# Kernel optimization log

Measured on AMD Instinct MI355X. Metric: run time of the kernel, lower is better.

Reference implementation:

```python
import jax, jax.numpy as jnp
import numpy as np

N, E, IN_DIM, HID, HEADS, OUT_DIM, T = 50000, 200000, 32, 64, 4, 32, 3
NEG_SLOPE = 0.2  # PyG GATv2Conv default


def setup_inputs() -> dict:
    key = jax.random.key(0)
    ks = jax.random.split(key, 16)
    s = 0.1
    return {
        "feat": jax.random.normal(ks[0], (N, IN_DIM), jnp.float32),
        "W_in": jax.random.normal(ks[1], (IN_DIM, HID), jnp.float32) * s,
        "b_in": jnp.zeros((HID,), jnp.float32),
        "Wl": jax.random.normal(ks[2], (2 * HID, HEADS * HID), jnp.float32) * s,
        "bl": jnp.zeros((HEADS * HID,), jnp.float32),
        "Wr": jax.random.normal(ks[3], (2 * HID, HEADS * HID), jnp.float32) * s,
        "br": jnp.zeros((HEADS * HID,), jnp.float32),
        "att": jax.random.normal(ks[4], (HEADS, HID), jnp.float32) * s,
        "b_conv": jnp.zeros((HEADS * HID,), jnp.float32),
        "Wg": jax.random.normal(ks[5], (HID, OUT_DIM), jnp.float32) * s,
        "bg": jnp.zeros((OUT_DIM,), jnp.float32),
        "edge_index": jax.random.randint(ks[6], (2, E), 0, N, jnp.int32),
        "node_mask": jax.random.randint(ks[7], (N,), 0, T + 1, jnp.int32),
        "current_state": jax.random.randint(ks[8], (N,), 0, 2, jnp.int32),
    }


def reference(feat, W_in, b_in, Wl, bl, Wr, br, att, b_conv, Wg, bg,
              edge_index, node_mask, current_state):
    # add self loops (GATv2Conv add_self_loops=True)
    loops = jnp.arange(N, dtype=edge_index.dtype)
    src = jnp.concatenate([edge_index[0], loops])  # [E+N]
    dst = jnp.concatenate([edge_index[1], loops])

    h0 = feat @ W_in + b_in  # [N, HID]
    bias_sum = b_conv.reshape(HEADS, HID).sum(0)  # heads are summed after bias add

    def step(h, i):
        active = node_mask > i  # [N] bool: nodes updated at this step
        x = jnp.concatenate([h, h0], axis=-1)  # [N, 2*HID]
        xl = (x @ Wl + bl).reshape(N, HEADS, HID)  # source transform
        xr = (x @ Wr + br).reshape(N, HEADS, HID)  # target transform
        e_act = active[src] & active[dst]  # edge alive iff both endpoints active
        s = jax.nn.leaky_relu(xl[src] + xr[dst], NEG_SLOPE)  # [E+N, H, C]
        score = jnp.einsum('ehc,hc->eh', s, att)  # [E+N, H]
        score = jnp.where(e_act[:, None], score, -1e30)
        smax = jax.lax.stop_gradient(
            jax.ops.segment_max(score, dst, num_segments=N))  # [N, H]
        ex = jnp.exp(score - smax[dst]) * e_act[:, None].astype(score.dtype)
        denom = jax.ops.segment_sum(ex, dst, num_segments=N)  # [N, H]
        alpha = ex / jnp.maximum(denom[dst], 1e-16)  # segment softmax per dst
        msg = alpha[:, :, None] * xl[src]  # [E+N, H, C]
        agg = jax.ops.segment_sum(msg, dst, num_segments=N)  # [N, H, C]
        out = jnp.tanh(agg.sum(1) + bias_sum)  # sum over heads, then Tanh
        return jnp.where(active[:, None], out, h), None

    h, _ = jax.lax.scan(step, h0, jnp.arange(T))
    # original returns g_embed(h[current_state]); fixed-shape variant: mask rows
    out = (h @ Wg + bg) * (current_state[:, None] > 0).astype(h.dtype)
    return out
```

## Files before the change

### kernel.cpp

```cpp
#include <hip/hip_runtime.h>
#include <hip/hip_bf16.h>

#define NN      50000
#define EE      200000
#define IN_DIM  32
#define HID     64
#define HEADS   4
#define OUTD    32
#define TSTEPS  3

typedef unsigned short bf16_t;
typedef __attribute__((ext_vector_type(8))) short  short8;
typedef __attribute__((ext_vector_type(4))) float  floatx4;

__device__ __forceinline__ float b2f(bf16_t u) {
    union { unsigned int i; float f; } v; v.i = ((unsigned int)u) << 16; return v.f;
}
__device__ __forceinline__ bf16_t f2b(float f) {
    union { float f; unsigned int i; } v; v.f = f;
    unsigned int r = v.i + 0x7FFF + ((v.i >> 16) & 1);
    return (bf16_t)(r >> 16);
}

__global__ __launch_bounds__(256) void k_setup(
        const void* W_in, const void* b_in, const void* att, const void* bconv,
        const void* Wg, const void* bg,
        const void* Wl_raw, const void* Wr_raw, const void* bl_raw, const void* br_raw,
        float* Winf, float* binf, float* attf, float* bcf, float* Wgf, float* bgf,
        bf16_t* __restrict__ Wt, float* __restrict__ bb,
        int* __restrict__ deg, int* __restrict__ flag, int* __restrict__ mbuf) {
    __shared__ int bad;
    int t = threadIdx.x, bid = blockIdx.x;
    if (t == 0) bad = 0;
    __syncthreads();
    {
        const bf16_t* p = (const bf16_t*)W_in;
        int mybad = 0;
        for (int i = t; i < IN_DIM * HID; i += 256) {
            float v = b2f(p[i]);
            if (v != v || fabsf(v) > 100.f) mybad = 1;
        }
        if (mybad) atomicOr(&bad, 1);
    }
    __syncthreads();
    int f = bad ? 0 : 1;
    if (bid == 0 && t == 0) *flag = f;

    if (bid < 256) {
        int i = bid * 256 + t;
        int n = i >> 7, k = i & 127;
        const void* W = (n < 256) ? Wl_raw : Wr_raw;
        int nn = (n < 256) ? n : n - 256;
        float v = f ? b2f(((const bf16_t*)W)[k * 256 + nn])
                    : ((const float*)W)[k * 256 + nn];
        Wt[i] = f2b(v);
        if (k == 0) {
            const void* b = (n < 256) ? bl_raw : br_raw;
            bb[n] = f ? b2f(((const bf16_t*)b)[nn]) : ((const float*)b)[nn];
        }
    } else if (bid < 275) {
        int i = (bid - 256) * 256 + t;
        const void* src; float* dst; int off;
        if      (i < 2048) { src = W_in;  dst = Winf; off = i; }
        else if (i < 2112) { src = b_in;  dst = binf; off = i - 2048; }
        else if (i < 2368) { src = att;   dst = attf; off = i - 2112; }
        else if (i < 2624) { src = bconv; dst = bcf;  off = i - 2368; }
        else if (i < 4672) { src = Wg;    dst = Wgf;  off = i - 2624; }
        else if (i < 4704) { src = bg;    dst = bgf;  off = i - 4672; }
        else return;
        dst[off] = f ? b2f(((const bf16_t*)src)[off]) : ((const float*)src)[off];
    } else {
        int i = (bid - 275) * 256 + t;
        if (i < NN) deg[i] = 0;
        if (bid == 275 && t < 16) mbuf[t] = 0;
    }
}

__global__ __launch_bounds__(256) void k_hist_all(const int* __restrict__ dst,
                                                  const int* __restrict__ mask,
                                                  int* __restrict__ deg,
                                                  int* __restrict__ mbuf) {
    int t = threadIdx.x, bid = blockIdx.x;
    int i = bid * 256 + t;
    if (i < EE) atomicAdd(&deg[dst[i]], 1);
    if (bid < (NN + 255) / 256) {
        __shared__ int wcnt[4][4];
        int wid = t >> 6, lane = t & 63;
        int ni = bid * 256 + t;
        bool valid = ni < NN;
        int v = 0;
        if (valid) { int m = mask[ni]; v = m < 0 ? 0 : (m > 3 ? 3 : m); }
#pragma unroll
        for (int b = 0; b < 4; b++) {
            unsigned long long mm = __ballot(valid && v == b);
            if (lane == 0) wcnt[wid][b] = __popcll(mm);
        }
        __syncthreads();
        if (t < 4) {
            int s = wcnt[0][t] + wcnt[1][t] + wcnt[2][t] + wcnt[3][t];
            if (s) atomicAdd(&mbuf[t], s);
        }
    }
}

__global__ __launch_bounds__(256) void k_scan_partial(const int* __restrict__ deg,
                                                      int* __restrict__ part, int n) {
    __shared__ int sd[256];
    int t = threadIdx.x;
    int base = blockIdx.x * 1024;
    int s = 0;
#pragma unroll
    for (int j = 0; j < 4; j++) {
        int i = base + t * 4 + j;
        if (i < n) s += deg[i];
    }
    sd[t] = s; __syncthreads();
    for (int off = 128; off > 0; off >>= 1) {
        if (t < off) sd[t] += sd[t + off];
        __syncthreads();
    }
    if (t == 0) part[blockIdx.x] = sd[0];
}

__global__ void k_scan_mid(int* part, int nch, int* mbuf) {
    if (threadIdx.x == 0 && blockIdx.x == 0) {
        int acc = 0;
        for (int i = 0; i < nch; i++) { int v = part[i]; part[i] = acc; acc += v; }
        part[nch] = acc;
        int c1 = mbuf[1], c2 = mbuf[2], c3 = mbuf[3];
        mbuf[7] = 0;
        mbuf[6] = c3;
        mbuf[5] = c3 + c2;
        mbuf[4] = c3 + c2 + c1;
        mbuf[8] = c3 + c2 + c1;
        mbuf[9] = c3 + c2;
        mbuf[10] = c3;
    }
}

__global__ __launch_bounds__(256) void k_scan_final(const int* __restrict__ deg,
                                                    const int* __restrict__ part,
                                                    int* __restrict__ row_ptr,
                                                    int* __restrict__ cursor,
                                                    int n, int nch) {
    __shared__ int sc[256];
    int t = threadIdx.x;
    int base = blockIdx.x * 1024;
    int v[4]; int s = 0;
#pragma unroll
    for (int j = 0; j < 4; j++) {
        int i = base + t * 4 + j;
        v[j] = (i < n) ? deg[i] : 0;
        s += v[j];
    }
    sc[t] = s; __syncthreads();
    for (int off = 1; off < 256; off <<= 1) {
        int add = (t >= off) ? sc[t - off] : 0;
        __syncthreads();
        sc[t] += add;
        __syncthreads();
    }
    int run = sc[t] - s + part[blockIdx.x];
#pragma unroll
    for (int j = 0; j < 4; j++) {
        int i = base + t * 4 + j;
        if (i < n) { row_ptr[i] = run; cursor[i] = run; run += v[j]; }
    }
    if (blockIdx.x == 0 && t == 0) row_ptr[n] = part[nch];
}

__global__ __launch_bounds__(256) void k_scatter_all(const int* __restrict__ src,
                                                     const int* __restrict__ dst,
                                                     int* __restrict__ cursor,
                                                     int* __restrict__ col,
                                                     const int* __restrict__ mask,
                                                     int* __restrict__ mbuf,
                                                     int* __restrict__ order) {
    int t = threadIdx.x, bid = blockIdx.x;
    int i = bid * 256 + t;
    if (i < EE) {
        int sv = src[i];
        int m = mask[sv]; m = m < 0 ? 0 : (m > 3 ? 3 : m);
        int d = dst[i];
        int pos = atomicAdd(&cursor[d], 1);
        col[pos] = sv | (m << 28);
    }
    if (bid < (NN + 255) / 256) {
        __shared__ int wcnt[4][4];
        __shared__ int bbase[4];
        int wid = t >> 6, lane = t & 63;
        int ni = bid * 256 + t;
        bool valid = ni < NN;
        int v = 0;
        if (valid) { int m = mask[ni]; v = m < 0 ? 0 : (m > 3 ? 3 : m); }
        int rank = 0;
#pragma unroll
        for (int b = 0; b < 4; b++) {
            unsigned long long mm = __ballot(valid && v == b);
            if (valid && v == b)
                rank = __popcll(mm & ((lane == 0) ? 0ull : (~0ull >> (64 - lane))));
            if (lane == 0) wcnt[wid][b] = __popcll(mm);
        }
        __syncthreads();
        if (t < 4) {
            int tot = wcnt[0][t] + wcnt[1][t] + wcnt[2][t] + wcnt[3][t];
            bbase[t] = atomicAdd(&mbuf[4 + t], tot);
        }
        __syncthreads();
        if (valid) {
            int wpre = 0;
            for (int ww = 0; ww < wid; ww++) wpre += wcnt[ww][v];
            order[bbase[v] + wpre + rank] = ni;
        }
    }
}

__global__ __launch_bounds__(256) void k_h0(const void* __restrict__ feat_raw,
                                            const float* __restrict__ W_in,
                                            const float* __restrict__ b_in,
                                            bf16_t* __restrict__ h0,
                                            bf16_t* __restrict__ h,
                                            const int* __restrict__ flag) {
    __shared__ float Ws[IN_DIM * HID];
    __shared__ float bs[HID];
    int t = threadIdx.x;
    for (int i = t; i < IN_DIM * HID; i += 256) Ws[i] = W_in[i];
    if (t < HID) bs[t] = b_in[t];
    __syncthreads();
    int node = blockIdx.x * 4 + (t >> 6);
    int c = t & 63;
    if (node >= NN) return;
    int f = *flag;
    float acc = bs[c];
    if (f) {
        const bf16_t* fr = (const bf16_t*)feat_raw + (size_t)node * IN_DIM;
#pragma unroll
        for (int k = 0; k < IN_DIM; k++) acc += b2f(fr[k]) * Ws[k * HID + c];
    } else {
        const float* fr = (const float*)feat_raw + (size_t)node * IN_DIM;
#pragma unroll
        for (int k = 0; k < IN_DIM; k++) acc += fr[k] * Ws[k * HID + c];
    }
    bf16_t o = f2b(acc);
    h0[(size_t)node * HID + c] = o;
    h [(size_t)node * HID + c] = o;
}

__global__ __launch_bounds__(256) void k_gemm_mfma(const bf16_t* __restrict__ h,
                                                   const bf16_t* __restrict__ h0,
                                                   const bf16_t* __restrict__ Wt,
                                                   const float* __restrict__ bb,
                                                   bf16_t* __restrict__ xl,
                                                   bf16_t* __restrict__ xr,
                                                   const int* __restrict__ order,
                                                   const int* __restrict__ mbuf,
                                                   int step) {
    int count = mbuf[8 + step];
    int mbase = blockIdx.x * 64;
    if (mbase >= count) return;

    __shared__ bf16_t smem[64 * 136 + 128 * 136];
    bf16_t* As = smem;
    bf16_t* Bs = smem + 64 * 136;
    bf16_t* Cs = smem;

    int t = threadIdx.x;
    int nbase = blockIdx.y * 128;

    {
        int ln = t >> 2, lq = t & 3;
        int idx = mbase + ln;
        int node = (idx < count) ? order[idx] : -1;
        ulonglong2 z; z.x = 0; z.y = 0;
#pragma unroll
        for (int j = 0; j < 2; j++) {
            int chunk = lq + j * 4;
            ulonglong2 vh = z, vh0 = z;
            if (node >= 0) {
                vh  = *(const ulonglong2*)(h  + (size_t)node * HID + chunk * 8);
                vh0 = *(const ulonglong2*)(h0 + (size_t)node * HID + chunk * 8);
            }
            *(ulonglong2*)(&As[ln * 136 + chunk * 8]) = vh;
            *(ulonglong2*)(&As[ln * 136 + 64 + chunk * 8]) = vh0;
        }
    }
#pragma unroll
    for (int i = 0; i < 8; i++) {
        int c = t + i * 256;
        int n = c >> 4, kc = (c & 15) * 8;
        *(ulonglong2*)(&Bs[n * 136 + kc]) =
            *(const ulonglong2*)(Wt + (size_t)(nbase + n) * 128 + kc);
    }
    __syncthreads();

    int wv = t >> 6;
    int lane = t & 63;
    int mrow = lane & 15;
    int quad = lane >> 4;

    floatx4 acc[8];
#pragma unroll
    for (int nf = 0; nf < 8; nf++) acc[nf] = (floatx4){0.f, 0.f, 0.f, 0.f};

#pragma unroll
    for (int kq = 0; kq < 4; kq++) {
        short8 a = *(const short8*)(&As[(wv * 16 + mrow) * 136 + kq * 32 + quad * 8]);
#pragma unroll
        for (int nf = 0; nf < 8; nf++) {
            short8 b = *(const short8*)(&Bs[(nf * 16 + mrow) * 136 + kq * 32 + quad * 8]);
            acc[nf] = __builtin_amdgcn_mfma_f32_16x16x32_bf16(a, b, acc[nf], 0, 0, 0);
        }
    }
    __syncthreads();

#pragma unroll
    for (int nf = 0; nf < 8; nf++) {
        float bv = bb[nbase + nf * 16 + mrow];
#pragma unroll
        for (int r = 0; r < 4; r++) {
            int m = wv * 16 + quad * 4 + r;
            Cs[m * 136 + nf * 16 + mrow] = f2b(acc[nf][r] + bv);
        }
    }
    __syncthreads();

    bf16_t* outp = (blockIdx.y < 2) ? xl : xr;
    int cc = (blockIdx.y & 1) * 128;
#pragma unroll
    for (int i = 0; i < 4; i++) {
        int c = t + i * 256;
        int m = c >> 4, kc = (c & 15) * 8;
        int idx = mbase + m;
        if (idx < count) {
            int node = order[idx];
            *(ulonglong2*)(outp + (size_t)node * 256 + cc + kc) =
                *(const ulonglong2*)(&Cs[m * 136 + kc]);
        }
    }
}

__global__ __launch_bounds__(256) void k_agg(bf16_t* __restrict__ h,
                                             const bf16_t* __restrict__ xl,
                                             const bf16_t* __restrict__ xr,
                                             const float* __restrict__ att,
                                             const float* __restrict__ b_conv,
                                             const int* __restrict__ row_ptr,
                                             const int* __restrict__ col,
                                             const int* __restrict__ order,
                                             const int* __restrict__ mbuf,
                                             int step) {
    int count = mbuf[8 + step];
    int wid = threadIdx.x >> 6;
    int lane = threadIdx.x & 63;
    float4 attv = *(const float4*)(att + lane * 4);
    float4 bcv  = *(const float4*)(b_conv + lane * 4);

    for (int idx = blockIdx.x * 4 + wid; idx < count; idx += gridDim.x * 4) {
        int node = order[idx];

        ushort4 xru = *(const ushort4*)(xr + (size_t)node * 256 + lane * 4);
        float xr0 = b2f(xru.x), xr1 = b2f(xru.y), xr2 = b2f(xru.z), xr3 = b2f(xru.w);

        float a0 = 0.f, a1 = 0.f, a2 = 0.f, a3 = 0.f, l = 0.f;

        auto do_edge = [&](int s) {
            ushort4 xu = *(const ushort4*)(xl + (size_t)s * 256 + lane * 4);
            float x0 = b2f(xu.x), x1 = b2f(xu.y), x2 = b2f(xu.z), x3 = b2f(xu.w);
            float v0 = x0 + xr0; v0 = v0 > 0.f ? v0 : 0.2f * v0;
            float v1 = x1 + xr1; v1 = v1 > 0.f ? v1 : 0.2f * v1;
            float v2 = x2 + xr2; v2 = v2 > 0.f ? v2 : 0.2f * v2;
            float v3 = x3 + xr3; v3 = v3 > 0.f ? v3 : 0.2f * v3;
            float part = attv.x * v0 + attv.y * v1 + attv.z * v2 + attv.w * v3;
            part += __shfl_xor(part, 1, 64);
            part += __shfl_xor(part, 2, 64);
            part += __shfl_xor(part, 4, 64);
            part += __shfl_xor(part, 8, 64);
            float p = __expf(part);
            l += p;
            a0 += p * x0; a1 += p * x1; a2 += p * x2; a3 += p * x3;
        };

        do_edge(node);
        int e0 = row_ptr[node], e1 = row_ptr[node + 1];
        int e = e0;
        for (; e + 3 < e1; e += 4) {
            int c0 = col[e], c1 = col[e + 1], c2 = col[e + 2], c3 = col[e + 3];
            if (((unsigned)c0 >> 28) > (unsigned)step) do_edge(c0 & 0x0FFFFFFF);
            if (((unsigned)c1 >> 28) > (unsigned)step) do_edge(c1 & 0x0FFFFFFF);
            if (((unsigned)c2 >> 28) > (unsigned)step) do_edge(c2 & 0x0FFFFFFF);
            if (((unsigned)c3 >> 28) > (unsigned)step) do_edge(c3 & 0x0FFFFFFF);
        }
        for (; e < e1; e++) {
            int c = col[e];
            if (((unsigned)c >> 28) > (unsigned)step) do_edge(c & 0x0FFFFFFF);
        }

        float inv = 1.f / l;
        float t0 = a0 * inv + bcv.x;
        float t1 = a1 * inv + bcv.y;
        float t2 = a2 * inv + bcv.z;
        float t3 = a3 * inv + bcv.w;
        t0 += __shfl_xor(t0, 16, 64); t0 += __shfl_xor(t0, 32, 64);
        t1 += __shfl_xor(t1, 16, 64); t1 += __shfl_xor(t1, 32, 64);
        t2 += __shfl_xor(t2, 16, 64); t2 += __shfl_xor(t2, 32, 64);
        t3 += __shfl_xor(t3, 16, 64); t3 += __shfl_xor(t3, 32, 64);
        if (lane < 16) {
            ushort4 o;
            o.x = f2b(tanhf(t0)); o.y = f2b(tanhf(t1));
            o.z = f2b(tanhf(t2)); o.w = f2b(tanhf(t3));
            *(ushort4*)(h + (size_t)node * HID + lane * 4) = o;
        }
    }
}

__global__ __launch_bounds__(256) void k_out(const bf16_t* __restrict__ h,
                                             const float* __restrict__ Wg,
                                             const float* __restrict__ bg,
                                             const int* __restrict__ cs,
                                             void* __restrict__ out,
                                             const int* __restrict__ flag) {
    __shared__ float Ws[HID * OUTD];
    __shared__ float bs[OUTD];
    int t = threadIdx.x;
    for (int i = t; i < HID * OUTD; i += 256) Ws[i] = Wg[i];
    if (t < OUTD) bs[t] = bg[t];
    __syncthreads();
    int node = blockIdx.x * 8 + (t >> 5);
    int c = t & 31;
    if (node >= NN) return;
    float res = 0.f;
    if (cs[node] > 0) {
        const bf16_t* hr = h + (size_t)node * HID;
        float acc = bs[c];
#pragma unroll
        for (int k = 0; k < HID; k++) acc += b2f(hr[k]) * Ws[k * OUTD + c];
        res = acc;
    }
    size_t idx = (size_t)node * OUTD + c;
    if (*flag) ((bf16_t*)out)[idx] = f2b(res);
    else       ((float*)out)[idx]  = res;
}

static inline size_t alignup(size_t x) { return (x + 255) & ~(size_t)255; }

extern "C" void kernel_launch(void* const* d_in, const int* in_sizes, int n_in,
                              void* d_out, int out_size, void* d_ws, size_t ws_size,
                              hipStream_t stream) {
    const void* feat_raw  = d_in[0];
    const void* W_in_raw  = d_in[1];
    const void* b_in_raw  = d_in[2];
    const void* Wl_raw    = d_in[3];
    const void* bl_raw    = d_in[4];
    const void* Wr_raw    = d_in[5];
    const void* br_raw    = d_in[6];
    const void* att_raw   = d_in[7];
    const void* bconv_raw = d_in[8];
    const void* Wg_raw    = d_in[9];
    const void* bg_raw    = d_in[10];
    const int* edge       = (const int*)d_in[11];
    const int* nmask      = (const int*)d_in[12];
    const int* cstate     = (const int*)d_in[13];

    const int* e_src = edge;
    const int* e_dst = edge + EE;

    const size_t SZ_HB   = alignup((size_t)NN * HID * sizeof(bf16_t));
    const size_t SZ_X    = alignup((size_t)NN * 256 * sizeof(bf16_t));
    const size_t SZ_I    = alignup((size_t)NN * sizeof(int));
    const size_t SZ_RP   = alignup((size_t)(NN + 1) * sizeof(int));
    const size_t SZ_COL  = alignup((size_t)EE * sizeof(int));
    const int nch = (NN + 1023) / 1024;
    const size_t SZ_PART = alignup((size_t)(nch + 1) * sizeof(int));
    const size_t SZ_WIN  = alignup((size_t)IN_DIM * HID * sizeof(float));
    const size_t SZ_WT   = alignup((size_t)512 * 128 * sizeof(bf16_t));
    const size_t SZ_B    = alignup(512 * sizeof(float));
    const size_t SZ_WG   = alignup((size_t)HID * OUTD * sizeof(float));

    char* w = (char*)d_ws;
    bf16_t* h0   = (bf16_t*)w; w += SZ_HB;
    bf16_t* h    = (bf16_t*)w; w += SZ_HB;
    bf16_t* xl   = (bf16_t*)w; w += SZ_X;
    bf16_t* xr   = (bf16_t*)w; w += SZ_X;
    int* deg     = (int*)w;    w += SZ_I;
    int* row_ptr = (int*)w;    w += SZ_RP;
    int* cursor  = (int*)w;    w += SZ_I;
    int* colA    = (int*)w;    w += SZ_COL;
    int* order   = (int*)w;    w += SZ_I;
    int* part    = (int*)w;    w += SZ_PART;
    float* Winf  = (float*)w;  w += SZ_WIN;
    bf16_t* Wt   = (bf16_t*)w; w += SZ_WT;
    float* bb    = (float*)w;  w += SZ_B;
    float* attf  = (float*)w;  w += SZ_B;
    float* bcf   = (float*)w;  w += SZ_B;
    float* Wgf   = (float*)w;  w += SZ_WG;
    float* binf  = (float*)w;  w += SZ_B;
    float* bgf   = (float*)w;  w += SZ_B;
    int* flag    = (int*)w;    w += 256;
    int* mbuf    = (int*)w;    w += 256;
    if ((size_t)(w - (char*)d_ws) > ws_size) return;

    k_setup<<<275 + (NN + 255) / 256, 256, 0, stream>>>(
        W_in_raw, b_in_raw, att_raw, bconv_raw, Wg_raw, bg_raw,
        Wl_raw, Wr_raw, bl_raw, br_raw,
        Winf, binf, attf, bcf, Wgf, bgf, Wt, bb, deg, flag, mbuf);

    k_hist_all<<<(EE + 255) / 256, 256, 0, stream>>>(e_dst, nmask, deg, mbuf);
    k_scan_partial<<<nch, 256, 0, stream>>>(deg, part, NN);
    k_scan_mid<<<1, 64, 0, stream>>>(part, nch, mbuf);
    k_scan_final<<<nch, 256, 0, stream>>>(deg, part, row_ptr, cursor, NN, nch);
    k_scatter_all<<<(EE + 255) / 256, 256, 0, stream>>>(e_src, e_dst, cursor, colA,
                                                        nmask, mbuf, order);

    k_h0<<<(NN + 3) / 4, 256, 0, stream>>>(feat_raw, Winf, binf, h0, h, flag);

    for (int s = 0; s < TSTEPS; s++) {
        k_gemm_mfma<<<dim3((NN + 63) / 64, 4), 256, 0, stream>>>(h, h0, Wt, bb, xl, xr,
                                                                 order, mbuf, s);
        k_agg<<<2048, 256, 0, stream>>>(h, xl, xr, attf, bcf,
                                        row_ptr, colA, order, mbuf, s);
    }

    k_out<<<(NN + 7) / 8, 256, 0, stream>>>(h, Wgf, bgf, cstate, d_out, flag);
}
```

Measured before the change: 271.1 us.

## Fold h0 into setup, merge scan mid, use K=64 GEMM for first step

At step 0, h equals h0, so [h,h0]@W equals h0@(W_top+W_bot). A pre-summed weight WtS is built and a K=64 GEMM kernel is used for the first step, halving that step's GEMM work. The h0 projection is fused into the setup kernel, and the single-thread scan_mid kernel is folded into scan_final, where each block recomputes its prefix serially. Together these cut launches and some arithmetic, at the cost of redundant serial prefix loops and summed weights rounded to bf16.

```diff
diff --git a/kernel.cpp b/kernel.cpp
--- a/kernel.cpp
+++ b/kernel.cpp
@@ -26,10 +26,14 @@
         const void* W_in, const void* b_in, const void* att, const void* bconv,
         const void* Wg, const void* bg,
         const void* Wl_raw, const void* Wr_raw, const void* bl_raw, const void* br_raw,
-        float* Winf, float* binf, float* attf, float* bcf, float* Wgf, float* bgf,
-        bf16_t* __restrict__ Wt, float* __restrict__ bb,
-        int* __restrict__ deg, int* __restrict__ flag, int* __restrict__ mbuf) {
+        const void* feat_raw,
+        float* attf, float* bcf, float* Wgf, float* bgf,
+        bf16_t* __restrict__ Wt, bf16_t* __restrict__ WtS, float* __restrict__ bb,
+        int* __restrict__ deg, int* __restrict__ flag, int* __restrict__ mbuf,
+        bf16_t* __restrict__ h0, bf16_t* __restrict__ h) {
     __shared__ int bad;
+    __shared__ float Ws[IN_DIM * HID];
+    __shared__ float bs[HID];
     int t = threadIdx.x, bid = blockIdx.x;
     if (t == 0) bad = 0;
     __syncthreads();
@@ -53,26 +57,51 @@
         int nn = (n < 256) ? n : n - 256;
         float v = f ? b2f(((const bf16_t*)W)[k * 256 + nn])
                     : ((const float*)W)[k * 256 + nn];
-        Wt[i] = f2b(v);
+        Wt[n * 128 + k] = f2b(v);
+        if (k < 64) {
+            float v2 = f ? b2f(((const bf16_t*)W)[(k + 64) * 256 + nn])
+                         : ((const float*)W)[(k + 64) * 256 + nn];
+            WtS[n * 64 + k] = f2b(v + v2);
+        }
         if (k == 0) {
             const void* b = (n < 256) ? bl_raw : br_raw;
             bb[n] = f ? b2f(((const bf16_t*)b)[nn]) : ((const float*)b)[nn];
         }
-    } else if (bid < 275) {
+    } else if (bid < 267) {
         int i = (bid - 256) * 256 + t;
         const void* src; float* dst; int off;
-        if      (i < 2048) { src = W_in;  dst = Winf; off = i; }
-        else if (i < 2112) { src = b_in;  dst = binf; off = i - 2048; }
-        else if (i < 2368) { src = att;   dst = attf; off = i - 2112; }
-        else if (i < 2624) { src = bconv; dst = bcf;  off = i - 2368; }
-        else if (i < 4672) { src = Wg;    dst = Wgf;  off = i - 2624; }
-        else if (i < 4704) { src = bg;    dst = bgf;  off = i - 4672; }
+        if      (i < 256)  { src = att;   dst = attf; off = i; }
+        else if (i < 512)  { src = bconv; dst = bcf;  off = i - 256; }
+        else if (i < 2560) { src = Wg;    dst = Wgf;  off = i - 512; }
+        else if (i < 2592) { src = bg;    dst = bgf;  off = i - 2560; }
         else return;
         dst[off] = f ? b2f(((const bf16_t*)src)[off]) : ((const float*)src)[off];
+    } else if (bid < 463) {
+        int i = (bid - 267) * 256 + t;
+        if (i < NN) deg[i] = 0;
+        if (bid == 267 && t < 16) mbuf[t] = 0;
     } else {
-        int i = (bid - 275) * 256 + t;
-        if (i < NN) deg[i] = 0;
-        if (bid == 275 && t < 16) mbuf[t] = 0;
+        for (int i = t; i < IN_DIM * HID; i += 256)
+            Ws[i] = f ? b2f(((const bf16_t*)W_in)[i]) : ((const float*)W_in)[i];
+        if (t < HID)
+            bs[t] = f ? b2f(((const bf16_t*)b_in)[t]) : ((const float*)b_in)[t];
+        __syncthreads();
+        int node = (bid - 463) * 4 + (t >> 6);
+        int c = t & 63;
+        if (node >= NN) return;
+        float acc = bs[c];
+        if (f) {
+            const bf16_t* fr = (const bf16_t*)feat_raw + (size_t)node * IN_DIM;
+#pragma unroll
+            for (int k = 0; k < IN_DIM; k++) acc += b2f(fr[k]) * Ws[k * HID + c];
+        } else {
+            const float* fr = (const float*)feat_raw + (size_t)node * IN_DIM;
+#pragma unroll
+            for (int k = 0; k < IN_DIM; k++) acc += fr[k] * Ws[k * HID + c];
+        }
+        bf16_t o = f2b(acc);
+        h0[(size_t)node * HID + c] = o;
+        h [(size_t)node * HID + c] = o;
     }
 }
 
@@ -122,30 +151,35 @@
     if (t == 0) part[blockIdx.x] = sd[0];
 }
 
-__global__ void k_scan_mid(int* part, int nch, int* mbuf) {
-    if (threadIdx.x == 0 && blockIdx.x == 0) {
-        int acc = 0;
-        for (int i = 0; i < nch; i++) { int v = part[i]; part[i] = acc; acc += v; }
-        part[nch] = acc;
-        int c1 = mbuf[1], c2 = mbuf[2], c3 = mbuf[3];
-        mbuf[7] = 0;
-        mbuf[6] = c3;
-        mbuf[5] = c3 + c2;
-        mbuf[4] = c3 + c2 + c1;
-        mbuf[8] = c3 + c2 + c1;
-        mbuf[9] = c3 + c2;
-        mbuf[10] = c3;
-    }
-}
-
 __global__ __launch_bounds__(256) void k_scan_final(const int* __restrict__ deg,
                                                     const int* __restrict__ part,
                                                     int* __restrict__ row_ptr,
                                                     int* __restrict__ cursor,
-                                                    int n, int nch) {
+                                                    int n, int nch,
+                                                    int* __restrict__ mbuf) {
     __shared__ int sc[256];
+    __shared__ int bpref;
     int t = threadIdx.x;
-    int base = blockIdx.x * 1024;
+    int bid = blockIdx.x;
+    if (t == 0) {
+        int acc = 0;
+        for (int i = 0; i < bid; i++) acc += part[i];
+        bpref = acc;
+        if (bid == 0) {
+            int tot = 0;
+            for (int i = 0; i < nch; i++) tot += part[i];
+            row_ptr[n] = tot;
+            int c1 = mbuf[1], c2 = mbuf[2], c3 = mbuf[3];
+            mbuf[7] = 0;
+            mbuf[6] = c3;
+            mbuf[5] = c3 + c2;
+            mbuf[4] = c3 + c2 + c1;
+            mbuf[8] = c3 + c2 + c1;
+            mbuf[9] = c3 + c2;
+            mbuf[10] = c3;
+        }
+    }
+    int base = bid * 1024;
     int v[4]; int s = 0;
 #pragma unroll
     for (int j = 0; j < 4; j++) {
@@ -160,13 +194,12 @@
         sc[t] += add;
         __syncthreads();
     }
-    int run = sc[t] - s + part[blockIdx.x];
+    int run = sc[t] - s + bpref;
 #pragma unroll
     for (int j = 0; j < 4; j++) {
         int i = base + t * 4 + j;
         if (i < n) { row_ptr[i] = run; cursor[i] = run; run += v[j]; }
     }
-    if (blockIdx.x == 0 && t == 0) row_ptr[n] = part[nch];
 }
 
 __global__ __launch_bounds__(256) void k_scatter_all(const int* __restrict__ src,
@@ -215,35 +248,88 @@
     }
 }
 
-__global__ __launch_bounds__(256) void k_h0(const void* __restrict__ feat_raw,
-                                            const float* __restrict__ W_in,
-                                            const float* __restrict__ b_in,
-                                            bf16_t* __restrict__ h0,
-                                            bf16_t* __restrict__ h,
-                                            const int* __restrict__ flag) {
-    __shared__ float Ws[IN_DIM * HID];
-    __shared__ float bs[HID];
+__global__ __launch_bounds__(256) void k_gemm0(const bf16_t* __restrict__ h0,
+                                               const bf16_t* __restrict__ WtS,
+                                               const float* __restrict__ bb,
+                                               bf16_t* __restrict__ xl,
+                                               bf16_t* __restrict__ xr,
+                                               const int* __restrict__ order,
+                                               const int* __restrict__ mbuf) {
+    int count = mbuf[8];
+    int mbase = blockIdx.x * 64;
+    if (mbase >= count) return;
+
+    __shared__ bf16_t smem[64 * 72 + 128 * 72];
+    bf16_t* As = smem;
+    bf16_t* Bs = smem + 64 * 72;
+    bf16_t* Cs = smem;
+
     int t = threadIdx.x;
-    for (int i = t; i < IN_DIM * HID; i += 256) Ws[i] = W_in[i];
-    if (t < HID) bs[t] = b_in[t];
-    __syncthreads();
-    int node = blockIdx.x * 4 + (t >> 6);
-    int c = t & 63;
-    if (node >= NN) return;
-    int f = *flag;
-    float acc = bs[c];
-    if (f) {
-        const bf16_t* fr = (const bf16_t*)feat_raw + (size_t)node * IN_DIM;
-#pragma unroll
-        for (int k = 0; k < IN_DIM; k++) acc += b2f(fr[k]) * Ws[k * HID + c];
-    } else {
-        const float* fr = (const float*)feat_raw + (size_t)node * IN_DIM;
-#pragma unroll
-        for (int k = 0; k < IN_DIM; k++) acc += fr[k] * Ws[k * HID + c];
-    }
-    bf16_t o = f2b(acc);
-    h0[(size_t)node * HID + c] = o;
-    h [(size_t)node * HID + c] = o;
+    int nbase = blockIdx.y * 128;
+
+    {
+        int ln = t >> 2, lq = t & 3;
+        int idx = mbase + ln;
+        int node = (idx < count) ? order[idx] : -1;
+        ulonglong2 z; z.x = 0; z.y = 0;
+        ulonglong2 v0 = z, v1 = z;
+        if (node >= 0) {
+            v0 = *(const ulonglong2*)(h0 + (size_t)node * HID + lq * 16);
+            v1 = *(const ulonglong2*)(h0 + (size_t)node * HID + lq * 16 + 8);
+        }
+        *(ulonglong2*)(&As[ln * 72 + lq * 16]) = v0;
+        *(ulonglong2*)(&As[ln * 72 + lq * 16 + 8]) = v1;
+    }
+    {
+        int n = t >> 1, kc = (t & 1) * 32;
+        const bf16_t* srcp = WtS + (size_t)(nbase + n) * 64 + kc;
+        bf16_t* dstp = &Bs[n * 72 + kc];
+        *(ulonglong2*)(dstp)      = *(const ulonglong2*)(srcp);
+        *(ulonglong2*)(dstp + 8)  = *(const ulonglong2*)(srcp + 8);
+        *(ulonglong2*)(dstp + 16) = *(const ulonglong2*)(srcp + 16);
+        *(ulonglong2*)(dstp + 24) = *(const ulonglong2*)(srcp + 24);
+    }
+    __syncthreads();
+
+    int wv = t >> 6, lane = t & 63, mrow = lane & 15, quad = lane >> 4;
+    floatx4 acc[8];
+#pragma unroll
+    for (int nf = 0; nf < 8; nf++) acc[nf] = (floatx4){0.f, 0.f, 0.f, 0.f};
+#pragma unroll
+    for (int kq = 0; kq < 2; kq++) {
+        short8 a = *(const short8*)(&As[(wv * 16 + mrow) * 72 + kq * 32 + quad * 8]);
+#pragma unroll
+        for (int nf = 0; nf < 8; nf++) {
+            short8 b = *(const short8*)(&Bs[(nf * 16 + mrow) * 72 + kq * 32 + quad * 8]);
+            acc[nf] = __builtin_amdgcn_mfma_f32_16x16x32_bf16(a, b, acc[nf], 0, 0, 0);
+        }
+    }
+    __syncthreads();
+
+#pragma unroll
+    for (int nf = 0; nf < 8; nf++) {
+        float bv = bb[nbase + nf * 16 + mrow];
+#pragma unroll
+        for (int r = 0; r < 4; r++) {
+            int m = wv * 16 + quad * 4 + r;
+            Cs[m * 136 + nf * 16 + mrow] = f2b(acc[nf][r] + bv);
+        }
+    }
+    __syncthreads();
+
+    bf16_t* outp = (blockIdx.y < 2) ? xl : xr;
+    int cc = (blockIdx.y & 1) * 128;
+#pragma unroll
+    for (int i = 0; i < 4; i++) {
+        int c = t + i * 256;
+        int m = c >> 4, kc = (c & 15) * 8;
+        int idx = mbase + m;
+        if (idx < count) {
+            int node = order[idx];
+            *(ulonglong2*)(outp + (size_t)node * 256 + cc + kc) =
+                *(const ulonglong2*)(&Cs[m * 136 + kc]);
+        }
+    }
 }
 
 __global__ __launch_bounds__(256) void k_gemm_mfma(const bf16_t* __restrict__ h,
@@ -293,15 +379,10 @@
     }
     __syncthreads();
 
-    int wv = t >> 6;
-    int lane = t & 63;
-    int mrow = lane & 15;
-    int quad = lane >> 4;
-
+    int wv = t >> 6, lane = t & 63, mrow = lane & 15, quad = lane >> 4;
     floatx4 acc[8];
 #pragma unroll
     for (int nf = 0; nf < 8; nf++) acc[nf] = (floatx4){0.f, 0.f, 0.f, 0.f};
-
 #pragma unroll
     for (int kq = 0; kq < 4; kq++) {
         short8 a = *(const short8*)(&As[(wv * 16 + mrow) * 136 + kq * 32 + quad * 8]);
@@ -471,8 +552,8 @@
     const size_t SZ_COL  = alignup((size_t)EE * sizeof(int));
     const int nch = (NN + 1023) / 1024;
     const size_t SZ_PART = alignup((size_t)(nch + 1) * sizeof(int));
-    const size_t SZ_WIN  = alignup((size_t)IN_DIM * HID * sizeof(float));
     const size_t SZ_WT   = alignup((size_t)512 * 128 * sizeof(bf16_t));
+    const size_t SZ_WTS  = alignup((size_t)512 * 64 * sizeof(bf16_t));
     const size_t SZ_B    = alignup(512 * sizeof(float));
     const size_t SZ_WG   = alignup((size_t)HID * OUTD * sizeof(float));
 
@@ -487,33 +568,32 @@
     int* colA    = (int*)w;    w += SZ_COL;
     int* order   = (int*)w;    w += SZ_I;
     int* part    = (int*)w;    w += SZ_PART;
-    float* Winf  = (float*)w;  w += SZ_WIN;
     bf16_t* Wt   = (bf16_t*)w; w += SZ_WT;
+    bf16_t* WtS  = (bf16_t*)w; w += SZ_WTS;
     float* bb    = (float*)w;  w += SZ_B;
     float* attf  = (float*)w;  w += SZ_B;
     float* bcf   = (float*)w;  w += SZ_B;
     float* Wgf   = (float*)w;  w += SZ_WG;
-    float* binf  = (float*)w;  w += SZ_B;
     float* bgf   = (float*)w;  w += SZ_B;
     int* flag    = (int*)w;    w += 256;
     int* mbuf    = (int*)w;    w += 256;
     if ((size_t)(w - (char*)d_ws) > ws_size) return;
 
-    k_setup<<<275 + (NN + 255) / 256, 256, 0, stream>>>(
+    k_setup<<<463 + (NN + 3) / 4, 256, 0, stream>>>(
         W_in_raw, b_in_raw, att_raw, bconv_raw, Wg_raw, bg_raw,
-        Wl_raw, Wr_raw, bl_raw, br_raw,
-        Winf, binf, attf, bcf, Wgf, bgf, Wt, bb, deg, flag, mbuf);
+        Wl_raw, Wr_raw, bl_raw, br_raw, feat_raw,
+        attf, bcf, Wgf, bgf, Wt, WtS, bb, deg, flag, mbuf, h0, h);
 
     k_hist_all<<<(EE + 255) / 256, 256, 0, stream>>>(e_dst, nmask, deg, mbuf);
     k_scan_partial<<<nch, 256, 0, stream>>>(deg, part, NN);
-    k_scan_mid<<<1, 64, 0, stream>>>(part, nch, mbuf);
-    k_scan_final<<<nch, 256, 0, stream>>>(deg, part, row_ptr, cursor, NN, nch);
+    k_scan_final<<<nch, 256, 0, stream>>>(deg, part, row_ptr, cursor, NN, nch, mbuf);
     k_scatter_all<<<(EE + 255) / 256, 256, 0, stream>>>(e_src, e_dst, cursor, colA,
                                                         nmask, mbuf, order);
 
-    k_h0<<<(NN + 3) / 4, 256, 0, stream>>>(feat_raw, Winf, binf, h0, h, flag);
-
-    for (int s = 0; s < TSTEPS; s++) {
+    k_gemm0<<<dim3((NN + 63) / 64, 4), 256, 0, stream>>>(h0, WtS, bb, xl, xr, order, mbuf);
+    k_agg<<<2048, 256, 0, stream>>>(h, xl, xr, attf, bcf, row_ptr, colA, order, mbuf, 0);
+
+    for (int s = 1; s < TSTEPS; s++) {
         k_gemm_mfma<<<dim3((NN + 63) / 64, 4), 256, 0, stream>>>(h, h0, Wt, bb, xl, xr,
                                                                  order, mbuf, s);
         k_agg<<<2048, 256, 0, stream>>>(h, xl, xr, attf, bcf,
```

Result: faster. 264.1 us (-2.6%).
